# Kernel optimization log

Measured on AMD Instinct MI355X. Metric: run time of the kernel, lower is better.

The kernel has to match this reference:

```python
import jax, jax.numpy as jnp
import numpy as np

EMBED = 1024
HEADS = 16
HEAD_DIM = EMBED // HEADS
SCALE = HEAD_DIM ** -0.5


def setup_inputs() -> dict:
    key = jax.random.key(0)
    ks = jax.random.split(key, 5)
    B, N = 2, 2048
    x = jax.random.normal(ks[0], (B, N, EMBED), dtype=jnp.float32)
    # qkv Linear: weight [3*EMBED, EMBED], bias [3*EMBED]
    w_qkv = jax.random.normal(ks[1], (3 * EMBED, EMBED), dtype=jnp.float32) * (EMBED ** -0.5)
    b_qkv = jnp.zeros((3 * EMBED,), dtype=jnp.float32)
    # proj Linear: weight [EMBED, EMBED], bias [EMBED]
    w_proj = jax.random.normal(ks[2], (EMBED, EMBED), dtype=jnp.float32) * (EMBED ** -0.5)
    b_proj = jnp.zeros((EMBED,), dtype=jnp.float32)
    return {"x": x, "w_qkv": w_qkv, "b_qkv": b_qkv, "w_proj": w_proj, "b_proj": b_proj}


def reference(x, w_qkv, b_qkv, w_proj, b_proj):
    B, N, _ = x.shape
    # QKV projection: [B, N, 3*EMBED]
    qkv = jnp.einsum('bnc,dc->bnd', x, w_qkv) + b_qkv
    qkv = qkv.reshape(B, N, 3, HEADS, HEAD_DIM).transpose(2, 0, 3, 1, 4)  # [3, B, H, N, Dh]
    q, k, v = qkv[0], qkv[1], qkv[2]
    # Explicit attention: matmul -> scale -> softmax -> matmul (eval mode, no dropout)
    attn = jnp.einsum('bhqd,bhkd->bhqk', q, k) * SCALE
    attn = jax.nn.softmax(attn, axis=-1)
    out = jnp.einsum('bhqk,bhkd->bhqd', attn, v)
    out = out.transpose(0, 2, 1, 3).reshape(B, N, EMBED)
    # Output projection (gamma1 is Identity; dropouts are zero in eval)
    out = jnp.einsum('bnc,dc->bnd', out, w_proj) + b_proj
    return out
```

## Files before the change

kernel.cpp:

```cpp
#include <hip/hip_runtime.h>
#include <stdint.h>

#define SEQ 2048

typedef __attribute__((ext_vector_type(8))) short bf16x8;
typedef __attribute__((ext_vector_type(4))) float f32x4;
typedef __attribute__((ext_vector_type(4))) int i32x4;

typedef const __attribute__((address_space(1))) unsigned int GVT;
typedef __attribute__((address_space(3))) unsigned int LVT;

static __device__ __forceinline__ unsigned short f2bf(float f) {
  unsigned u = __builtin_bit_cast(unsigned, f);
  u += 0x7fffu + ((u >> 16) & 1u);
  return (unsigned short)(u >> 16);
}

static __device__ __forceinline__ unsigned pk_bf16(float lo, float hi) {
  unsigned r;
  asm("v_cvt_pk_bf16_f32 %0, %1, %2" : "=v"(r) : "v"(lo), "v"(hi));
  return r;
}

__global__ __launch_bounds__(256) void cvt3_kernel(
    const float* __restrict__ s0, unsigned short* __restrict__ d0, int n0,
    const float* __restrict__ s1, unsigned short* __restrict__ d1, int n1,
    const float* __restrict__ s2, unsigned short* __restrict__ d2, int n2) {
  int i = blockIdx.x * 256 + threadIdx.x;
  const int stride = gridDim.x * 256;
  const int total = n0 + n1 + n2;
  for (; i < total; i += stride) {
    const float* s;
    unsigned short* d;
    int k;
    if (i < n0) { s = s0; d = d0; k = i; }
    else if (i < n0 + n1) { s = s1; d = d1; k = i - n0; }
    else { s = s2; d = d2; k = i - n0 - n1; }
    float4 v = reinterpret_cast<const float4*>(s)[k];
    ushort4 o;
    o.x = f2bf(v.x); o.y = f2bf(v.y); o.z = f2bf(v.z); o.w = f2bf(v.w);
    reinterpret_cast<ushort4*>(d)[k] = o;
  }
}

__global__ __launch_bounds__(256, 2) void gemm_qkv_kernel(
    const unsigned short* __restrict__ A,
    const unsigned short* __restrict__ Bt,
    const float* __restrict__ bias,
    unsigned short* __restrict__ qb,
    unsigned short* __restrict__ kbuf,
    unsigned short* __restrict__ vtbuf) {
  __shared__ __align__(16) unsigned short As[2][128 * 32];
  __shared__ __align__(16) unsigned short Bs[2][128 * 32];
  const int tid = threadIdx.x;
  const int lane = tid & 63;
  const int wid = tid >> 6;
  const int wr = wid >> 1, wc = wid & 1;
  const int lin = blockIdx.y * 24 + blockIdx.x;
  const int wg = (lin & 7) * 96 + (lin >> 3);
  const int bm = wg / 24, bn = wg % 24;
  const int lr = lane & 15, hg = lane >> 4;

  f32x4 acc[4][4] = {};

  const int r0 = tid >> 2;
  const int c0 = (tid & 3) * 8;

  auto STAGE = [&](int b, int kt) {
    const unsigned short* ga0 = A + (size_t)(bm * 128 + r0) * 1024 + kt * 32 + c0;
    const unsigned short* ga1 = A + (size_t)(bm * 128 + r0 + 64) * 1024 + kt * 32 + c0;
    const unsigned short* gb0 = Bt + (size_t)(bn * 128 + r0) * 1024 + kt * 32 + c0;
    const unsigned short* gb1 = Bt + (size_t)(bn * 128 + r0 + 64) * 1024 + kt * 32 + c0;
    __builtin_amdgcn_global_load_lds((GVT*)ga0, (LVT*)&As[b][tid * 8], 16, 0, 0);
    __builtin_amdgcn_global_load_lds((GVT*)ga1, (LVT*)&As[b][(tid + 256) * 8], 16, 0, 0);
    __builtin_amdgcn_global_load_lds((GVT*)gb0, (LVT*)&Bs[b][tid * 8], 16, 0, 0);
    __builtin_amdgcn_global_load_lds((GVT*)gb1, (LVT*)&Bs[b][(tid + 256) * 8], 16, 0, 0);
  };

  STAGE(0, 0);
  int cur = 0;
  for (int kt = 0; kt < 32; ++kt) {
    __syncthreads();
    if (kt + 1 < 32) STAGE(cur ^ 1, kt + 1);
    bf16x8 af[4], bfr[4];
#pragma unroll
    for (int i = 0; i < 4; ++i) {
      af[i] = *reinterpret_cast<const bf16x8*>(&As[cur][(wr * 64 + i * 16 + lr) * 32 + hg * 8]);
      bfr[i] = *reinterpret_cast<const bf16x8*>(&Bs[cur][(wc * 64 + i * 16 + lr) * 32 + hg * 8]);
    }
    __builtin_amdgcn_s_setprio(1);
#pragma unroll
    for (int i = 0; i < 4; ++i)
#pragma unroll
      for (int j = 0; j < 4; ++j)
        acc[i][j] = __builtin_amdgcn_mfma_f32_16x16x32_bf16(af[i], bfr[j], acc[i][j], 0, 0, 0);
    __builtin_amdgcn_s_setprio(0);
    cur ^= 1;
  }

#pragma unroll
  for (int j = 0; j < 4; ++j) {
    const int col = bn * 128 + wc * 64 + j * 16 + lr;
    const float bv = bias[col];
    const int which = col >> 10;
    const int hh = (col >> 6) & 15;
    const int dh = col & 63;
    const float scl = which == 0 ? 0.18033688011112042f : 1.0f;
#pragma unroll
    for (int i = 0; i < 4; ++i) {
      if (which == 2) {
        const int row0 = bm * 128 + wr * 64 + i * 16 + hg * 4;
        const int b = row0 >> 11, n0 = row0 & 2047;
        ushort4 vv;
        vv.x = f2bf(acc[i][j][0] + bv);
        vv.y = f2bf(acc[i][j][1] + bv);
        vv.z = f2bf(acc[i][j][2] + bv);
        vv.w = f2bf(acc[i][j][3] + bv);
        *reinterpret_cast<ushort4*>(
            &vtbuf[((size_t)((b * 16 + hh) * 64 + dh)) * 2048 + n0]) = vv;
      } else {
        unsigned short* dst = which == 0 ? qb : kbuf;
#pragma unroll
        for (int r = 0; r < 4; ++r) {
          const int row = bm * 128 + wr * 64 + i * 16 + hg * 4 + r;
          const int b = row >> 11, n = row & 2047;
          dst[((size_t)((b * 16 + hh) * 2048 + n)) * 64 + dh] = f2bf((acc[i][j][r] + bv) * scl);
        }
      }
    }
  }
}

__global__ __launch_bounds__(256, 2) void gemm_proj_kernel(
    const unsigned short* __restrict__ A,
    const unsigned short* __restrict__ Bt,
    const float* __restrict__ bias,
    float* __restrict__ out) {
  __shared__ __align__(16) unsigned short As[2][128 * 32];
  __shared__ __align__(16) unsigned short Bs[2][128 * 32];
  const int tid = threadIdx.x;
  const int lane = tid & 63;
  const int wid = tid >> 6;
  const int wr = wid >> 1, wc = wid & 1;
  const int lin = blockIdx.y * 8 + blockIdx.x;
  const int wg = (lin & 7) * 32 + (lin >> 3);
  const int bm = wg / 8, bn = wg % 8;
  const int lr = lane & 15, hg = lane >> 4;

  f32x4 acc[4][4] = {};
  const int r0 = tid >> 2;
  const int c0 = (tid & 3) * 8;

  auto STAGE = [&](int b, int kt) {
    const unsigned short* ga0 = A + (size_t)(bm * 128 + r0) * 1024 + kt * 32 + c0;
    const unsigned short* ga1 = A + (size_t)(bm * 128 + r0 + 64) * 1024 + kt * 32 + c0;
    const unsigned short* gb0 = Bt + (size_t)(bn * 128 + r0) * 1024 + kt * 32 + c0;
    const unsigned short* gb1 = Bt + (size_t)(bn * 128 + r0 + 64) * 1024 + kt * 32 + c0;
    __builtin_amdgcn_global_load_lds((GVT*)ga0, (LVT*)&As[b][tid * 8], 16, 0, 0);
    __builtin_amdgcn_global_load_lds((GVT*)ga1, (LVT*)&As[b][(tid + 256) * 8], 16, 0, 0);
    __builtin_amdgcn_global_load_lds((GVT*)gb0, (LVT*)&Bs[b][tid * 8], 16, 0, 0);
    __builtin_amdgcn_global_load_lds((GVT*)gb1, (LVT*)&Bs[b][(tid + 256) * 8], 16, 0, 0);
  };

  STAGE(0, 0);
  int cur = 0;
  for (int kt = 0; kt < 32; ++kt) {
    __syncthreads();
    if (kt + 1 < 32) STAGE(cur ^ 1, kt + 1);
    bf16x8 af[4], bfr[4];
#pragma unroll
    for (int i = 0; i < 4; ++i) {
      af[i] = *reinterpret_cast<const bf16x8*>(&As[cur][(wr * 64 + i * 16 + lr) * 32 + hg * 8]);
      bfr[i] = *reinterpret_cast<const bf16x8*>(&Bs[cur][(wc * 64 + i * 16 + lr) * 32 + hg * 8]);
    }
    __builtin_amdgcn_s_setprio(1);
#pragma unroll
    for (int i = 0; i < 4; ++i)
#pragma unroll
      for (int j = 0; j < 4; ++j)
        acc[i][j] = __builtin_amdgcn_mfma_f32_16x16x32_bf16(af[i], bfr[j], acc[i][j], 0, 0, 0);
    __builtin_amdgcn_s_setprio(0);
    cur ^= 1;
  }

#pragma unroll
  for (int j = 0; j < 4; ++j) {
    const int col = bn * 128 + wc * 64 + j * 16 + lr;
    const float bv = bias[col];
#pragma unroll
    for (int i = 0; i < 4; ++i)
#pragma unroll
      for (int r = 0; r < 4; ++r) {
        const int row = bm * 128 + wr * 64 + i * 16 + hg * 4 + r;
        out[(size_t)row * 1024 + col] = acc[i][j][r] + bv;
      }
  }
}

__global__ __launch_bounds__(256, 2) void attn_kernel(
    const unsigned short* __restrict__ qb,
    const unsigned short* __restrict__ kbuf,
    const unsigned short* __restrict__ vt,
    unsigned short* __restrict__ ao) {
  __shared__ __align__(16) unsigned short Ks[2][64 * 64];
  __shared__ __align__(16) unsigned short Vs[2][64 * 64];
  const int tid = threadIdx.x;
  const int lane = tid & 63;
  const int wid = tid >> 6;
  const int lr = lane & 15;
  const int hg = lane >> 4;
  const int lin = blockIdx.y * 16 + blockIdx.x;
  const int wg = (lin & 7) * 64 + (lin >> 3);
  const int qt = wg & 15;
  const int bh = wg >> 4;
  const size_t hbase = (size_t)bh * SEQ * 64;

  bf16x8 qf[2][2];
#pragma unroll
  for (int m = 0; m < 2; ++m) {
    const unsigned short* qp =
        qb + hbase + (size_t)(qt * 128 + wid * 32 + m * 16 + lr) * 64 + hg * 8;
    qf[m][0] = *reinterpret_cast<const bf16x8*>(qp);
    qf[m][1] = *reinterpret_cast<const bf16x8*>(qp + 32);
  }

  f32x4 accO[2][4] = {};
  float m_run[2] = {-1e30f, -1e30f};
  float l_run[2] = {0.0f, 0.0f};

  auto STAGE = [&](int b, int kt) {
#pragma unroll
    for (int c = 0; c < 2; ++c) {
      const int t = tid + c * 256;
      const int row = t >> 3;
      const int sw = ((t & 7) ^ (row & 7)) * 8;
      const unsigned short* gk = kbuf + hbase + (size_t)(kt * 64 + row) * 64 + sw;
      __builtin_amdgcn_global_load_lds((GVT*)gk, (LVT*)&Ks[b][t * 8], 16, 0, 0);
      const unsigned short* gv = vt + hbase + (size_t)row * 2048 + kt * 64 + sw;
      __builtin_amdgcn_global_load_lds((GVT*)gv, (LVT*)&Vs[b][t * 8], 16, 0, 0);
    }
  };

  STAGE(0, 0);
  int cur = 0;
  const int sw0 = (hg ^ (lr & 7)) * 8;
  const int sw1 = ((hg + 4) ^ (lr & 7)) * 8;

  for (int kt = 0; kt < 32; ++kt) {
    __syncthreads();
    if (kt + 1 < 32) STAGE(cur ^ 1, kt + 1);

    f32x4 accT[2][4] = {};
    __builtin_amdgcn_s_setprio(1);
#pragma unroll
    for (int j = 0; j < 4; ++j) {
      const bf16x8 kf0 = *reinterpret_cast<const bf16x8*>(&Ks[cur][(j * 16 + lr) * 64 + sw0]);
      const bf16x8 kf1 = *reinterpret_cast<const bf16x8*>(&Ks[cur][(j * 16 + lr) * 64 + sw1]);
      accT[0][j] = __builtin_amdgcn_mfma_f32_16x16x32_bf16(kf0, qf[0][0], accT[0][j], 0, 0, 0);
      accT[0][j] = __builtin_amdgcn_mfma_f32_16x16x32_bf16(kf1, qf[0][1], accT[0][j], 0, 0, 0);
      accT[1][j] = __builtin_amdgcn_mfma_f32_16x16x32_bf16(kf0, qf[1][0], accT[1][j], 0, 0, 0);
      accT[1][j] = __builtin_amdgcn_mfma_f32_16x16x32_bf16(kf1, qf[1][1], accT[1][j], 0, 0, 0);
    }
    __builtin_amdgcn_s_setprio(0);

    bf16x8 pB[2][2];
#pragma unroll
    for (int m = 0; m < 2; ++m) {
      float t0 = fmaxf(fmaxf(accT[m][0][0], accT[m][0][1]), fmaxf(accT[m][0][2], accT[m][0][3]));
      float t1 = fmaxf(fmaxf(accT[m][1][0], accT[m][1][1]), fmaxf(accT[m][1][2], accT[m][1][3]));
      float t2 = fmaxf(fmaxf(accT[m][2][0], accT[m][2][1]), fmaxf(accT[m][2][2], accT[m][2][3]));
      float t3 = fmaxf(fmaxf(accT[m][3][0], accT[m][3][1]), fmaxf(accT[m][3][2], accT[m][3][3]));
      float mt = fmaxf(fmaxf(t0, t1), fmaxf(t2, t3));
      mt = fmaxf(mt, __shfl_xor(mt, 16));
      mt = fmaxf(mt, __shfl_xor(mt, 32));
      if (__any(mt > m_run[m] + 8.0f)) {
        const float mnew = fmaxf(m_run[m], mt);
        const float crr = __builtin_amdgcn_exp2f(m_run[m] - mnew);
        m_run[m] = mnew;
        l_run[m] *= crr;
#pragma unroll
        for (int jd = 0; jd < 4; ++jd)
#pragma unroll
          for (int r = 0; r < 4; ++r) accO[m][jd][r] *= crr;
      }
      unsigned w[4][2];
      float ps0 = 0.f, ps1 = 0.f;
#pragma unroll
      for (int j = 0; j < 4; ++j) {
        const float p0 = __builtin_amdgcn_exp2f(accT[m][j][0] - m_run[m]);
        const float p1 = __builtin_amdgcn_exp2f(accT[m][j][1] - m_run[m]);
        const float p2 = __builtin_amdgcn_exp2f(accT[m][j][2] - m_run[m]);
        const float p3 = __builtin_amdgcn_exp2f(accT[m][j][3] - m_run[m]);
        ps0 += (p0 + p1);
        ps1 += (p2 + p3);
        w[j][0] = pk_bf16(p0, p1);
        w[j][1] = pk_bf16(p2, p3);
      }
      float ps = ps0 + ps1;
      ps += __shfl_xor(ps, 16);
      ps += __shfl_xor(ps, 32);
      l_run[m] += ps;
#pragma unroll
      for (int h = 0; h < 2; ++h) {
        unsigned e0 = w[2 * h][0], e1 = w[2 * h][1];
        unsigned f0 = w[2 * h + 1][0], f1 = w[2 * h + 1][1];
        asm("v_permlane32_swap_b32 %0, %1" : "+v"(e0), "+v"(f0));
        asm("v_permlane32_swap_b32 %0, %1" : "+v"(e1), "+v"(f1));
        asm("v_permlane16_swap_b32 %0, %1" : "+v"(e0), "+v"(f0));
        asm("v_permlane16_swap_b32 %0, %1" : "+v"(e1), "+v"(f1));
        const i32x4 pw = {(int)e0, (int)e1, (int)f0, (int)f1};
        pB[m][h] = __builtin_bit_cast(bf16x8, pw);
      }
    }

    __builtin_amdgcn_s_setprio(1);
#pragma unroll
    for (int jd = 0; jd < 4; ++jd) {
      const bf16x8 v0 = *reinterpret_cast<const bf16x8*>(&Vs[cur][(jd * 16 + lr) * 64 + sw0]);
      const bf16x8 v1 = *reinterpret_cast<const bf16x8*>(&Vs[cur][(jd * 16 + lr) * 64 + sw1]);
      accO[0][jd] = __builtin_amdgcn_mfma_f32_16x16x32_bf16(v0, pB[0][0], accO[0][jd], 0, 0, 0);
      accO[0][jd] = __builtin_amdgcn_mfma_f32_16x16x32_bf16(v1, pB[0][1], accO[0][jd], 0, 0, 0);
      accO[1][jd] = __builtin_amdgcn_mfma_f32_16x16x32_bf16(v0, pB[1][0], accO[1][jd], 0, 0, 0);
      accO[1][jd] = __builtin_amdgcn_mfma_f32_16x16x32_bf16(v1, pB[1][1], accO[1][jd], 0, 0, 0);
    }
    __builtin_amdgcn_s_setprio(0);
    cur ^= 1;
  }

  const int b = bh >> 4, hh = bh & 15;
#pragma unroll
  for (int m = 0; m < 2; ++m) {
    const float invl = 1.0f / l_run[m];
    const int qrow = qt * 128 + wid * 32 + m * 16 + lr;
    unsigned short* dst = ao + (size_t)(b * 2048 + qrow) * 1024 + hh * 64;
#pragma unroll
    for (int jd = 0; jd < 4; ++jd) {
      uint2 o;
      o.x = pk_bf16(accO[m][jd][0] * invl, accO[m][jd][1] * invl);
      o.y = pk_bf16(accO[m][jd][2] * invl, accO[m][jd][3] * invl);
      *reinterpret_cast<uint2*>(dst + jd * 16 + hg * 4) = o;
    }
  }
}

extern "C" void kernel_launch(void* const* d_in, const int* in_sizes, int n_in,
                              void* d_out, int out_size, void* d_ws, size_t ws_size,
                              hipStream_t stream) {
  const float* x = (const float*)d_in[0];
  const float* w_qkv = (const float*)d_in[1];
  const float* b_qkv = (const float*)d_in[2];
  const float* w_proj = (const float*)d_in[3];
  const float* b_proj = (const float*)d_in[4];
  float* out = (float*)d_out;
  char* ws = (char*)d_ws;
  unsigned short* x_bf = (unsigned short*)(ws);
  unsigned short* ao_bf = (unsigned short*)(ws);
  unsigned short* wq_bf = (unsigned short*)(ws + (8ull << 20));
  unsigned short* wp_bf = (unsigned short*)(ws + (14ull << 20));
  unsigned short* q_bf = (unsigned short*)(ws + (16ull << 20));
  unsigned short* k_bf = (unsigned short*)(ws + (24ull << 20));
  unsigned short* vt_bf = (unsigned short*)(ws + (32ull << 20));

  cvt3_kernel<<<2048, 256, 0, stream>>>(x, x_bf, 4096 * 1024 / 4,
                                        w_qkv, wq_bf, 3072 * 1024 / 4,
                                        w_proj, wp_bf, 1024 * 1024 / 4);
  gemm_qkv_kernel<<<dim3(24, 32), 256, 0, stream>>>(x_bf, wq_bf, b_qkv, q_bf, k_bf, vt_bf);
  attn_kernel<<<dim3(16, 32), 256, 0, stream>>>(q_bf, k_bf, vt_bf, ao_bf);
  gemm_proj_kernel<<<dim3(8, 32), 256, 0, stream>>>(ao_bf, wp_bf, b_proj, out);
}
```

Baseline: 130.4 us.

## Split attention block into 8 waves with 16 query rows each

The attention kernel now launches 512 threads per block, so each of 8 waves handles 16 query rows instead of 32. Each thread issues one K/V staging load per tile instead of two. This halves per-wave register state (accumulators, softmax stats) to allow higher occupancy and more latency hiding. In exchange, each K/V fragment read from LDS is reused by half as many MFMAs, which doubles LDS read traffic per FLOP and adds barrier cost across more waves.

```diff
diff --git a/kernel.cpp b/kernel.cpp
--- a/kernel.cpp
+++ b/kernel.cpp
@@ -197,7 +197,7 @@
   }
 }
 
-__global__ __launch_bounds__(256, 2) void attn_kernel(
+__global__ __launch_bounds__(512, 4) void attn_kernel(
     const unsigned short* __restrict__ qb,
     const unsigned short* __restrict__ kbuf,
     const unsigned short* __restrict__ vt,
@@ -215,30 +215,25 @@
   const int bh = wg >> 4;
   const size_t hbase = (size_t)bh * SEQ * 64;
 
-  bf16x8 qf[2][2];
-#pragma unroll
-  for (int m = 0; m < 2; ++m) {
+  bf16x8 qf[2];
+  {
     const unsigned short* qp =
-        qb + hbase + (size_t)(qt * 128 + wid * 32 + m * 16 + lr) * 64 + hg * 8;
-    qf[m][0] = *reinterpret_cast<const bf16x8*>(qp);
-    qf[m][1] = *reinterpret_cast<const bf16x8*>(qp + 32);
-  }
-
-  f32x4 accO[2][4] = {};
-  float m_run[2] = {-1e30f, -1e30f};
-  float l_run[2] = {0.0f, 0.0f};
+        qb + hbase + (size_t)(qt * 128 + wid * 16 + lr) * 64 + hg * 8;
+    qf[0] = *reinterpret_cast<const bf16x8*>(qp);
+    qf[1] = *reinterpret_cast<const bf16x8*>(qp + 32);
+  }
+
+  f32x4 accO[4] = {};
+  float m_run = -1e30f;
+  float l_run = 0.0f;
 
   auto STAGE = [&](int b, int kt) {
-#pragma unroll
-    for (int c = 0; c < 2; ++c) {
-      const int t = tid + c * 256;
-      const int row = t >> 3;
-      const int sw = ((t & 7) ^ (row & 7)) * 8;
-      const unsigned short* gk = kbuf + hbase + (size_t)(kt * 64 + row) * 64 + sw;
-      __builtin_amdgcn_global_load_lds((GVT*)gk, (LVT*)&Ks[b][t * 8], 16, 0, 0);
-      const unsigned short* gv = vt + hbase + (size_t)row * 2048 + kt * 64 + sw;
-      __builtin_amdgcn_global_load_lds((GVT*)gv, (LVT*)&Vs[b][t * 8], 16, 0, 0);
-    }
+    const int row = tid >> 3;
+    const int sw = ((tid & 7) ^ (row & 7)) * 8;
+    const unsigned short* gk = kbuf + hbase + (size_t)(kt * 64 + row) * 64 + sw;
+    __builtin_amdgcn_global_load_lds((GVT*)gk, (LVT*)&Ks[b][tid * 8], 16, 0, 0);
+    const unsigned short* gv = vt + hbase + (size_t)row * 2048 + kt * 64 + sw;
+    __builtin_amdgcn_global_load_lds((GVT*)gv, (LVT*)&Vs[b][tid * 8], 16, 0, 0);
   };
 
   STAGE(0, 0);
@@ -250,47 +245,44 @@
     __syncthreads();
     if (kt + 1 < 32) STAGE(cur ^ 1, kt + 1);
 
-    f32x4 accT[2][4] = {};
+    f32x4 accT[4] = {};
     __builtin_amdgcn_s_setprio(1);
 #pragma unroll
     for (int j = 0; j < 4; ++j) {
       const bf16x8 kf0 = *reinterpret_cast<const bf16x8*>(&Ks[cur][(j * 16 + lr) * 64 + sw0]);
       const bf16x8 kf1 = *reinterpret_cast<const bf16x8*>(&Ks[cur][(j * 16 + lr) * 64 + sw1]);
-      accT[0][j] = __builtin_amdgcn_mfma_f32_16x16x32_bf16(kf0, qf[0][0], accT[0][j], 0, 0, 0);
-      accT[0][j] = __builtin_amdgcn_mfma_f32_16x16x32_bf16(kf1, qf[0][1], accT[0][j], 0, 0, 0);
-      accT[1][j] = __builtin_amdgcn_mfma_f32_16x16x32_bf16(kf0, qf[1][0], accT[1][j], 0, 0, 0);
-      accT[1][j] = __builtin_amdgcn_mfma_f32_16x16x32_bf16(kf1, qf[1][1], accT[1][j], 0, 0, 0);
+      accT[j] = __builtin_amdgcn_mfma_f32_16x16x32_bf16(kf0, qf[0], accT[j], 0, 0, 0);
+      accT[j] = __builtin_amdgcn_mfma_f32_16x16x32_bf16(kf1, qf[1], accT[j], 0, 0, 0);
     }
     __builtin_amdgcn_s_setprio(0);
 
-    bf16x8 pB[2][2];
-#pragma unroll
-    for (int m = 0; m < 2; ++m) {
-      float t0 = fmaxf(fmaxf(accT[m][0][0], accT[m][0][1]), fmaxf(accT[m][0][2], accT[m][0][3]));
-      float t1 = fmaxf(fmaxf(accT[m][1][0], accT[m][1][1]), fmaxf(accT[m][1][2], accT[m][1][3]));
-      float t2 = fmaxf(fmaxf(accT[m][2][0], accT[m][2][1]), fmaxf(accT[m][2][2], accT[m][2][3]));
-      float t3 = fmaxf(fmaxf(accT[m][3][0], accT[m][3][1]), fmaxf(accT[m][3][2], accT[m][3][3]));
+    bf16x8 pB[2];
+    {
+      float t0 = fmaxf(fmaxf(accT[0][0], accT[0][1]), fmaxf(accT[0][2], accT[0][3]));
+      float t1 = fmaxf(fmaxf(accT[1][0], accT[1][1]), fmaxf(accT[1][2], accT[1][3]));
+      float t2 = fmaxf(fmaxf(accT[2][0], accT[2][1]), fmaxf(accT[2][2], accT[2][3]));
+      float t3 = fmaxf(fmaxf(accT[3][0], accT[3][1]), fmaxf(accT[3][2], accT[3][3]));
       float mt = fmaxf(fmaxf(t0, t1), fmaxf(t2, t3));
       mt = fmaxf(mt, __shfl_xor(mt, 16));
       mt = fmaxf(mt, __shfl_xor(mt, 32));
-      if (__any(mt > m_run[m] + 8.0f)) {
-        const float mnew = fmaxf(m_run[m], mt);
-        const float crr = __builtin_amdgcn_exp2f(m_run[m] - mnew);
-        m_run[m] = mnew;
-        l_run[m] *= crr;
+      if (__any(mt > m_run + 8.0f)) {
+        const float mnew = fmaxf(m_run, mt);
+        const float crr = __builtin_amdgcn_exp2f(m_run - mnew);
+        m_run = mnew;
+        l_run *= crr;
 #pragma unroll
         for (int jd = 0; jd < 4; ++jd)
 #pragma unroll
-          for (int r = 0; r < 4; ++r) accO[m][jd][r] *= crr;
+          for (int r = 0; r < 4; ++r) accO[jd][r] *= crr;
       }
       unsigned w[4][2];
       float ps0 = 0.f, ps1 = 0.f;
 #pragma unroll
       for (int j = 0; j < 4; ++j) {
-        const float p0 = __builtin_amdgcn_exp2f(accT[m][j][0] - m_run[m]);
-        const float p1 = __builtin_amdgcn_exp2f(accT[m][j][1] - m_run[m]);
-        const float p2 = __builtin_amdgcn_exp2f(accT[m][j][2] - m_run[m]);
-        const float p3 = __builtin_amdgcn_exp2f(accT[m][j][3] - m_run[m]);
+        const float p0 = __builtin_amdgcn_exp2f(accT[j][0] - m_run);
+        const float p1 = __builtin_amdgcn_exp2f(accT[j][1] - m_run);
+        const float p2 = __builtin_amdgcn_exp2f(accT[j][2] - m_run);
+        const float p3 = __builtin_amdgcn_exp2f(accT[j][3] - m_run);
         ps0 += (p0 + p1);
         ps1 += (p2 + p3);
         w[j][0] = pk_bf16(p0, p1);
@@ -299,7 +291,7 @@
       float ps = ps0 + ps1;
       ps += __shfl_xor(ps, 16);
       ps += __shfl_xor(ps, 32);
-      l_run[m] += ps;
+      l_run += ps;
 #pragma unroll
       for (int h = 0; h < 2; ++h) {
         unsigned e0 = w[2 * h][0], e1 = w[2 * h][1];
@@ -309,7 +301,7 @@
         asm("v_permlane16_swap_b32 %0, %1" : "+v"(e0), "+v"(f0));
         asm("v_permlane16_swap_b32 %0, %1" : "+v"(e1), "+v"(f1));
         const i32x4 pw = {(int)e0, (int)e1, (int)f0, (int)f1};
-        pB[m][h] = __builtin_bit_cast(bf16x8, pw);
+        pB[h] = __builtin_bit_cast(bf16x8, pw);
       }
     }
 
@@ -318,26 +310,23 @@
     for (int jd = 0; jd < 4; ++jd) {
       const bf16x8 v0 = *reinterpret_cast<const bf16x8*>(&Vs[cur][(jd * 16 + lr) * 64 + sw0]);
       const bf16x8 v1 = *reinterpret_cast<const bf16x8*>(&Vs[cur][(jd * 16 + lr) * 64 + sw1]);
-      accO[0][jd] = __builtin_amdgcn_mfma_f32_16x16x32_bf16(v0, pB[0][0], accO[0][jd], 0, 0, 0);
-      accO[0][jd] = __builtin_amdgcn_mfma_f32_16x16x32_bf16(v1, pB[0][1], accO[0][jd], 0, 0, 0);
-      accO[1][jd] = __builtin_amdgcn_mfma_f32_16x16x32_bf16(v0, pB[1][0], accO[1][jd], 0, 0, 0);
-      accO[1][jd] = __builtin_amdgcn_mfma_f32_16x16x32_bf16(v1, pB[1][1], accO[1][jd], 0, 0, 0);
+      accO[jd] = __builtin_amdgcn_mfma_f32_16x16x32_bf16(v0, pB[0], accO[jd], 0, 0, 0);
+      accO[jd] = __builtin_amdgcn_mfma_f32_16x16x32_bf16(v1, pB[1], accO[jd], 0, 0, 0);
     }
     __builtin_amdgcn_s_setprio(0);
     cur ^= 1;
   }
 
   const int b = bh >> 4, hh = bh & 15;
-#pragma unroll
-  for (int m = 0; m < 2; ++m) {
-    const float invl = 1.0f / l_run[m];
-    const int qrow = qt * 128 + wid * 32 + m * 16 + lr;
+  {
+    const float invl = 1.0f / l_run;
+    const int qrow = qt * 128 + wid * 16 + lr;
     unsigned short* dst = ao + (size_t)(b * 2048 + qrow) * 1024 + hh * 64;
 #pragma unroll
     for (int jd = 0; jd < 4; ++jd) {
       uint2 o;
-      o.x = pk_bf16(accO[m][jd][0] * invl, accO[m][jd][1] * invl);
-      o.y = pk_bf16(accO[m][jd][2] * invl, accO[m][jd][3] * invl);
+      o.x = pk_bf16(accO[jd][0] * invl, accO[jd][1] * invl);
+      o.y = pk_bf16(accO[jd][2] * invl, accO[jd][3] * invl);
       *reinterpret_cast<uint2*>(dst + jd * 16 + hg * 4) = o;
     }
   }
@@ -365,6 +354,6 @@
                                         w_qkv, wq_bf, 3072 * 1024 / 4,
                                         w_proj, wp_bf, 1024 * 1024 / 4);
   gemm_qkv_kernel<<<dim3(24, 32), 256, 0, stream>>>(x_bf, wq_bf, b_qkv, q_bf, k_bf, vt_bf);
-  attn_kernel<<<dim3(16, 32), 256, 0, stream>>>(q_bf, k_bf, vt_bf, ao_bf);
+  attn_kernel<<<dim3(16, 32), 512, 0, stream>>>(q_bf, k_bf, vt_bf, ao_bf);
   gemm_proj_kernel<<<dim3(8, 32), 256, 0, stream>>>(ao_bf, wp_bf, b_proj, out);
 }
```

Result: faster. 125.6 us (-3.7%).

## Split attention KV sequence across two wave groups and merge softmax states

Applied to the files above, without the earlier changes.

The attention kernel now runs 512 threads per block. Two groups of four waves each process half of the 2048 keys for the same 128 query rows, then combine their partial outputs through LDS with a flash-decoding style max/sum merge. This doubles the waves per query tile and halves the serial KV loop length, which is meant to raise occupancy and latency hiding. The cost is an extra LDS reduction and sync at the end. Launch bounds on the two GEMM kernels are also raised from 2 to 3 blocks per CU, which may constrain registers.

```diff
diff --git a/kernel.cpp b/kernel.cpp
--- a/kernel.cpp
+++ b/kernel.cpp
@@ -43,7 +43,7 @@
   }
 }
 
-__global__ __launch_bounds__(256, 2) void gemm_qkv_kernel(
+__global__ __launch_bounds__(256, 3) void gemm_qkv_kernel(
     const unsigned short* __restrict__ A,
     const unsigned short* __restrict__ Bt,
     const float* __restrict__ bias,
@@ -131,7 +131,7 @@
   }
 }
 
-__global__ __launch_bounds__(256, 2) void gemm_proj_kernel(
+__global__ __launch_bounds__(256, 3) void gemm_proj_kernel(
     const unsigned short* __restrict__ A,
     const unsigned short* __restrict__ Bt,
     const float* __restrict__ bias,
@@ -197,16 +197,17 @@
   }
 }
 
-__global__ __launch_bounds__(256, 2) void attn_kernel(
+__global__ __launch_bounds__(512, 4) void attn_kernel(
     const unsigned short* __restrict__ qb,
     const unsigned short* __restrict__ kbuf,
     const unsigned short* __restrict__ vt,
     unsigned short* __restrict__ ao) {
-  __shared__ __align__(16) unsigned short Ks[2][64 * 64];
-  __shared__ __align__(16) unsigned short Vs[2][64 * 64];
+  __shared__ __align__(16) unsigned short KVbuf[2][2][2][4096];
   const int tid = threadIdx.x;
   const int lane = tid & 63;
   const int wid = tid >> 6;
+  const int ws = wid >> 2;
+  const int wq = wid & 3;
   const int lr = lane & 15;
   const int hg = lane >> 4;
   const int lin = blockIdx.y * 16 + blockIdx.x;
@@ -219,7 +220,7 @@
 #pragma unroll
   for (int m = 0; m < 2; ++m) {
     const unsigned short* qp =
-        qb + hbase + (size_t)(qt * 128 + wid * 32 + m * 16 + lr) * 64 + hg * 8;
+        qb + hbase + (size_t)(qt * 128 + wq * 32 + m * 16 + lr) * 64 + hg * 8;
     qf[m][0] = *reinterpret_cast<const bf16x8*>(qp);
     qf[m][1] = *reinterpret_cast<const bf16x8*>(qp + 32);
   }
@@ -228,16 +229,17 @@
   float m_run[2] = {-1e30f, -1e30f};
   float l_run[2] = {0.0f, 0.0f};
 
+  const int srow = tid >> 3;
+  const int ssw = ((tid & 7) ^ (srow & 7)) * 8;
   auto STAGE = [&](int b, int kt) {
 #pragma unroll
-    for (int c = 0; c < 2; ++c) {
-      const int t = tid + c * 256;
-      const int row = t >> 3;
-      const int sw = ((t & 7) ^ (row & 7)) * 8;
-      const unsigned short* gk = kbuf + hbase + (size_t)(kt * 64 + row) * 64 + sw;
-      __builtin_amdgcn_global_load_lds((GVT*)gk, (LVT*)&Ks[b][t * 8], 16, 0, 0);
-      const unsigned short* gv = vt + hbase + (size_t)row * 2048 + kt * 64 + sw;
-      __builtin_amdgcn_global_load_lds((GVT*)gv, (LVT*)&Vs[b][t * 8], 16, 0, 0);
+    for (int s = 0; s < 2; ++s) {
+      const unsigned short* gk =
+          kbuf + hbase + (size_t)(s * 1024 + kt * 64 + srow) * 64 + ssw;
+      __builtin_amdgcn_global_load_lds((GVT*)gk, (LVT*)&KVbuf[0][s][b][tid * 8], 16, 0, 0);
+      const unsigned short* gv =
+          vt + hbase + (size_t)srow * 2048 + s * 1024 + kt * 64 + ssw;
+      __builtin_amdgcn_global_load_lds((GVT*)gv, (LVT*)&KVbuf[1][s][b][tid * 8], 16, 0, 0);
     }
   };
 
@@ -246,16 +248,19 @@
   const int sw0 = (hg ^ (lr & 7)) * 8;
   const int sw1 = ((hg + 4) ^ (lr & 7)) * 8;
 
-  for (int kt = 0; kt < 32; ++kt) {
+  for (int kt = 0; kt < 16; ++kt) {
     __syncthreads();
-    if (kt + 1 < 32) STAGE(cur ^ 1, kt + 1);
+    if (kt + 1 < 16) STAGE(cur ^ 1, kt + 1);
+
+    const unsigned short* Ksb = &KVbuf[0][ws][cur][0];
+    const unsigned short* Vsb = &KVbuf[1][ws][cur][0];
 
     f32x4 accT[2][4] = {};
     __builtin_amdgcn_s_setprio(1);
 #pragma unroll
     for (int j = 0; j < 4; ++j) {
-      const bf16x8 kf0 = *reinterpret_cast<const bf16x8*>(&Ks[cur][(j * 16 + lr) * 64 + sw0]);
-      const bf16x8 kf1 = *reinterpret_cast<const bf16x8*>(&Ks[cur][(j * 16 + lr) * 64 + sw1]);
+      const bf16x8 kf0 = *reinterpret_cast<const bf16x8*>(&Ksb[(j * 16 + lr) * 64 + sw0]);
+      const bf16x8 kf1 = *reinterpret_cast<const bf16x8*>(&Ksb[(j * 16 + lr) * 64 + sw1]);
       accT[0][j] = __builtin_amdgcn_mfma_f32_16x16x32_bf16(kf0, qf[0][0], accT[0][j], 0, 0, 0);
       accT[0][j] = __builtin_amdgcn_mfma_f32_16x16x32_bf16(kf1, qf[0][1], accT[0][j], 0, 0, 0);
       accT[1][j] = __builtin_amdgcn_mfma_f32_16x16x32_bf16(kf0, qf[1][0], accT[1][j], 0, 0, 0);
@@ -316,8 +321,8 @@
     __builtin_amdgcn_s_setprio(1);
 #pragma unroll
     for (int jd = 0; jd < 4; ++jd) {
-      const bf16x8 v0 = *reinterpret_cast<const bf16x8*>(&Vs[cur][(jd * 16 + lr) * 64 + sw0]);
-      const bf16x8 v1 = *reinterpret_cast<const bf16x8*>(&Vs[cur][(jd * 16 + lr) * 64 + sw1]);
+      const bf16x8 v0 = *reinterpret_cast<const bf16x8*>(&Vsb[(jd * 16 + lr) * 64 + sw0]);
+      const bf16x8 v1 = *reinterpret_cast<const bf16x8*>(&Vsb[(jd * 16 + lr) * 64 + sw1]);
       accO[0][jd] = __builtin_amdgcn_mfma_f32_16x16x32_bf16(v0, pB[0][0], accO[0][jd], 0, 0, 0);
       accO[0][jd] = __builtin_amdgcn_mfma_f32_16x16x32_bf16(v1, pB[0][1], accO[0][jd], 0, 0, 0);
       accO[1][jd] = __builtin_amdgcn_mfma_f32_16x16x32_bf16(v0, pB[1][0], accO[1][jd], 0, 0, 0);
@@ -327,18 +332,44 @@
     cur ^= 1;
   }
 
-  const int b = bh >> 4, hh = bh & 15;
-#pragma unroll
-  for (int m = 0; m < 2; ++m) {
-    const float invl = 1.0f / l_run[m];
-    const int qrow = qt * 128 + wid * 32 + m * 16 + lr;
-    unsigned short* dst = ao + (size_t)(b * 2048 + qrow) * 1024 + hh * 64;
-#pragma unroll
-    for (int jd = 0; jd < 4; ++jd) {
-      uint2 o;
-      o.x = pk_bf16(accO[m][jd][0] * invl, accO[m][jd][1] * invl);
-      o.y = pk_bf16(accO[m][jd][2] * invl, accO[m][jd][3] * invl);
-      *reinterpret_cast<uint2*>(dst + jd * 16 + hg * 4) = o;
+  float* scr = (float*)&KVbuf[0][0][0][0];
+  const int sbase = (wq * 64 + lane) * 37;
+  __syncthreads();
+  if (ws == 1) {
+#pragma unroll
+    for (int m = 0; m < 2; ++m) {
+#pragma unroll
+      for (int jd = 0; jd < 4; ++jd)
+#pragma unroll
+        for (int r = 0; r < 4; ++r) scr[sbase + m * 16 + jd * 4 + r] = accO[m][jd][r];
+      scr[sbase + 32 + m] = m_run[m];
+      scr[sbase + 34 + m] = l_run[m];
+    }
+  }
+  __syncthreads();
+  if (ws == 0) {
+    const int b = bh >> 4, hh = bh & 15;
+#pragma unroll
+    for (int m = 0; m < 2; ++m) {
+      const float pm = scr[sbase + 32 + m];
+      const float pl = scr[sbase + 34 + m];
+      const float mn = fmaxf(m_run[m], pm);
+      const float c1 = __builtin_amdgcn_exp2f(m_run[m] - mn);
+      const float c2 = __builtin_amdgcn_exp2f(pm - mn);
+      const float inv = 1.0f / (l_run[m] * c1 + pl * c2);
+      const int qrow = qt * 128 + wq * 32 + m * 16 + lr;
+      unsigned short* dst = ao + (size_t)(b * 2048 + qrow) * 1024 + hh * 64;
+#pragma unroll
+      for (int jd = 0; jd < 4; ++jd) {
+        const float o0 = (accO[m][jd][0] * c1 + scr[sbase + m * 16 + jd * 4 + 0] * c2) * inv;
+        const float o1 = (accO[m][jd][1] * c1 + scr[sbase + m * 16 + jd * 4 + 1] * c2) * inv;
+        const float o2 = (accO[m][jd][2] * c1 + scr[sbase + m * 16 + jd * 4 + 2] * c2) * inv;
+        const float o3 = (accO[m][jd][3] * c1 + scr[sbase + m * 16 + jd * 4 + 3] * c2) * inv;
+        uint2 o;
+        o.x = pk_bf16(o0, o1);
+        o.y = pk_bf16(o2, o3);
+        *reinterpret_cast<uint2*>(dst + jd * 16 + hg * 4) = o;
+      }
     }
   }
 }
@@ -365,6 +396,6 @@
                                         w_qkv, wq_bf, 3072 * 1024 / 4,
                                         w_proj, wp_bf, 1024 * 1024 / 4);
   gemm_qkv_kernel<<<dim3(24, 32), 256, 0, stream>>>(x_bf, wq_bf, b_qkv, q_bf, k_bf, vt_bf);
-  attn_kernel<<<dim3(16, 32), 256, 0, stream>>>(q_bf, k_bf, vt_bf, ao_bf);
+  attn_kernel<<<dim3(16, 32), 512, 0, stream>>>(q_bf, k_bf, vt_bf, ao_bf);
   gemm_proj_kernel<<<dim3(8, 32), 256, 0, stream>>>(ao_bf, wp_bf, b_proj, out);
 }
```

Result: faster. 120.5 us (-7.6%).
